# Kernel tuning notes

Hardware: AMD Instinct MI355X
Metric: run time of the kernel (lower is better)

The kernel has to match this reference:

```python
import jax, jax.numpy as jnp
import numpy as np

BN_EPS = 1e-5

# Binary activation with hardtanh STE semantics (forward: sign)
@jax.custom_vjp
def binary_act(x):
    return jnp.sign(x)

def _ba_fwd(x):
    return jnp.sign(x), x

def _ba_bwd(x, g):
    return (jnp.where(jnp.abs(x) > 1.0, 0.0, g),)

binary_act.defvjp(_ba_fwd, _ba_bwd)

# Binary weight quantizer (forward: sign, backward: identity STE)
@jax.custom_vjp
def binary_w(x):
    return jnp.sign(x)

def _bw_fwd(x):
    return jnp.sign(x), None

def _bw_bwd(_, g):
    return (g,)

binary_w.defvjp(_bw_fwd, _bw_bwd)


def setup_inputs() -> dict:
    key = jax.random.key(0)
    k1, k2, k3 = jax.random.split(key, 3)
    B, C_in, H, W_sp = 32, 256, 56, 56
    C_out, KH, KW = 256, 3, 3
    x = jax.random.normal(k1, (B, C_in, H, W_sp), dtype=jnp.float32)
    weight = jax.random.normal(k2, (C_out, C_in, KH, KW), dtype=jnp.float32) * 0.05
    bias = jax.random.normal(k3, (C_out,), dtype=jnp.float32) * 0.01
    gamma = jnp.ones((C_out,), dtype=jnp.float32)
    beta = jnp.zeros((C_out,), dtype=jnp.float32)
    return {"x": x, "weight": weight, "bias": bias, "gamma": gamma, "beta": beta}


def reference(x, weight, bias, gamma, beta):
    # --- activation binarization (A=2): sign ---
    xb = binary_act(x)
    # --- weight binarization (W=2): mean-center over in-channel dim, clamp, sign * alpha ---
    wc = weight - jnp.mean(weight, axis=1, keepdims=True)
    wc = jnp.clip(wc, -1.0, 1.0)
    alpha = jnp.mean(jnp.abs(wc), axis=(1, 2, 3), keepdims=True)  # per-output-channel scale
    wq = binary_w(wc) * alpha
    # --- conv2d, stride 1, padding 1 ---
    y = jax.lax.conv_general_dilated(
        xb, wq, window_strides=(1, 1), padding=((1, 1), (1, 1)),
        dimension_numbers=("NCHW", "OIHW", "NCHW"))
    y = y + bias[None, :, None, None]
    # --- BatchNorm2d (training-mode batch statistics, biased variance) ---
    mu = jnp.mean(y, axis=(0, 2, 3), keepdims=True)
    var = jnp.var(y, axis=(0, 2, 3), keepdims=True)
    y = (y - mu) * jax.lax.rsqrt(var + BN_EPS)
    y = y * gamma[None, :, None, None] + beta[None, :, None, None]
    # --- last_relu=1 ---
    y = jax.nn.relu(y)
    # --- last_bin=1 (A=2 -> binary activation) ---
    y = binary_act(y)
    return y
```

## Files before the change

kernel.cpp:

```cpp
#include <hip/hip_runtime.h>

typedef unsigned long long u64;
typedef int i32x4 __attribute__((ext_vector_type(4)));
typedef int i32x16 __attribute__((ext_vector_type(16)));

#define N_SP 3136
#define C_IN 256
#define C_OUT 256
#define BATCH 32
#define NBLK 896
#define XROW 64
#define XPLANE (58 * XROW * 256)
#define XSIZE ((size_t)BATCH * XPLANE)

__global__ __launch_bounds__(256) void prep_weights(const float* __restrict__ w,
                                                    char* __restrict__ A_pack,
                                                    double* __restrict__ alpha) {
    const int o = blockIdx.x;
    const int i = threadIdx.x;
    const int lane = i & 63, wvid = i >> 6;
    __shared__ double part[4][9];
    __shared__ double part2[4];

    float wv[9];
    const float* wp = w + ((size_t)o * C_IN + i) * 9;
#pragma unroll
    for (int t = 0; t < 9; ++t) wv[t] = wp[t];

#pragma unroll
    for (int t = 0; t < 9; ++t) {
        double v = (double)wv[t];
#pragma unroll
        for (int off = 32; off > 0; off >>= 1) v += __shfl_down(v, off);
        if (lane == 0) part[wvid][t] = v;
    }
    __syncthreads();

    double asum = 0.0;
#pragma unroll
    for (int t = 0; t < 9; ++t) {
        double mean = (part[0][t] + part[1][t] + part[2][t] + part[3][t]) * (1.0 / 256.0);
        double wc = (double)wv[t] - mean;
        int idx16 = ((t * 8 + (i >> 5)) * 8 + (o >> 5)) * 64 + (((i >> 4) & 1) << 5) + (o & 31);
        A_pack[(size_t)idx16 * 16 + (i & 15)] = (char)(wc > 0.0 ? 1 : -1);
        double aw = fabs(wc);
        if (aw > 1.0) aw = 1.0;
        asum += aw;
    }
#pragma unroll
    for (int off = 32; off > 0; off >>= 1) asum += __shfl_down(asum, off);
    if (lane == 0) part2[wvid] = asum;
    __syncthreads();
    if (i == 0)
        alpha[o] = (part2[0] + part2[1] + part2[2] + part2[3]) * (1.0 / 2304.0);
}

__global__ __launch_bounds__(256) void sign_transpose(const float* __restrict__ x,
                                                      char* __restrict__ xsT) {
    const int sp0 = blockIdx.x * 64;
    const int b = blockIdx.y;
    const int lane = threadIdx.x & 63;
    const int wv = threadIdx.x >> 6;
    __shared__ char tile[64 * 272];

    {
        const int tidl = (blockIdx.y * 49 + blockIdx.x) * 256 + threadIdx.x;
        if (tidl < 294912) {
            const int bb = tidl / 9216;
            const int r = tidl - bb * 9216;
            int hp, wp, c16;
            if (r < 2048) {
                hp = (r >> 10) * 57;
                wp = (r >> 4) & 63;
                c16 = (r & 15) << 4;
            } else {
                int r2 = r - 2048;
                hp = 1 + (r2 >> 7);
                int q = r2 & 127;
                int wi = q >> 4;
                wp = (wi == 0) ? 0 : 56 + wi;
                c16 = (q & 15) << 4;
            }
            *(i32x4*)(xsT + (((size_t)(bb * 58 + hp) << 6) + wp) * 256 + c16) =
                (i32x4){0, 0, 0, 0};
        }
    }

    const float* xp = x + ((size_t)(b * 256 + (wv << 6))) * N_SP + sp0 + lane;
#pragma unroll
    for (int q = 0; q < 4; ++q) {
        unsigned d[4];
#pragma unroll
        for (int dd = 0; dd < 4; ++dd) {
            unsigned v = 0;
#pragma unroll
            for (int kk = 0; kk < 4; ++kk) {
                int ci_l = (q << 4) + (dd << 2) + kk;
                float xv = xp[(size_t)ci_l * N_SP];
                v |= (unsigned)(xv > 0.0f ? 0x01u : 0xFFu) << (8 * kk);
            }
            d[dd] = v;
        }
        *(i32x4*)(tile + lane * 272 + (wv << 6) + (q << 4)) =
            (i32x4){(int)d[0], (int)d[1], (int)d[2], (int)d[3]};
    }
    __syncthreads();

    const int t = threadIdx.x;
#pragma unroll
    for (int j = 0; j < 4; ++j) {
        int sp_loc = (j << 4) + (t >> 4);
        int ci0 = (t & 15) << 4;
        i32x4 v = *(const i32x4*)(tile + sp_loc * 272 + ci0);
        int spg = sp0 + sp_loc;
        int h = spg / 56, w = spg - h * 56;
        size_t dst = (((size_t)(b * 58 + h + 1) << 6) + (w + 1)) * 256 + ci0;
        *(i32x4*)(xsT + dst) = v;
    }
}

__global__ __launch_bounds__(256, 2) void conv_mfma(const char* __restrict__ xsT,
                                                    const char* __restrict__ A_pack,
                                                    float* __restrict__ out,
                                                    int2* __restrict__ partials) {
    const int tid = threadIdx.x;
    const int lane = tid & 63;
    const int wv = tid >> 6;
    const int l31 = lane & 31, l5 = lane >> 5;
    const int blk = blockIdx.x;
    const int b = blk / 28;
    const int h0 = (blk - b * 28) * 2;

    __shared__ char slab[4 * 58 * 272];

    {
        const char* src = xsT + ((size_t)(b * 58 + h0) << 6) * 256;
        for (int c = tid; c < 4 * 58 * 16; c += 256) {
            int dh = c / (58 * 16);
            int rem = c - dh * (58 * 16);
            int wp = rem >> 4, c16 = (rem & 15) << 4;
            *(i32x4*)(slab + (dh * 58 + wp) * 272 + c16) =
                *(const i32x4*)(src + (size_t)dh * (XROW * 256) + wp * 256 + c16);
        }
    }
    __syncthreads();

    i32x16 acc[2][2][2] = {};

    const char* apb = A_pack + ((size_t)(2 * wv * 64 + lane)) * 16;
    const char* sb0 = slab + l31 * 272 + l5 * 16;
    int w1_0 = 32 + l31;     if (w1_0 > 57) w1_0 = 57;
    int w1_1 = 33 + l31;     if (w1_1 > 57) w1_1 = 57;
    int w1_2 = 34 + l31;     if (w1_2 > 57) w1_2 = 57;
    const char* sb1_0 = slab + w1_0 * 272 + l5 * 16;
    const char* sb1_1 = slab + w1_1 * 272 + l5 * 16;
    const char* sb1_2 = slab + w1_2 * 272 + l5 * 16;

#pragma unroll
    for (int tap = 0; tap < 9; ++tap) {
        const int dh = tap / 3, dw = tap - 3 * (tap / 3);
        const char* sb1 = (dw == 0) ? sb1_0 : ((dw == 1) ? sb1_1 : sb1_2);
#pragma unroll
        for (int cib = 0; cib < 8; ++cib) {
            const int it = tap * 8 + cib;
            i32x4 a0 = *(const i32x4*)(apb + (size_t)it * 8192);
            i32x4 a1 = *(const i32x4*)(apb + (size_t)it * 8192 + 1024);
            i32x4 b00 = *(const i32x4*)(sb0 + ((dh + 0) * 58 + dw) * 272 + cib * 32);
            i32x4 b01 = *(const i32x4*)(sb0 + ((dh + 1) * 58 + dw) * 272 + cib * 32);
            i32x4 b10 = *(const i32x4*)(sb1 + (dh + 0) * 58 * 272 + cib * 32);
            i32x4 b11 = *(const i32x4*)(sb1 + (dh + 1) * 58 * 272 + cib * 32);
            acc[0][0][0] = __builtin_amdgcn_mfma_i32_32x32x32_i8(a0, b00, acc[0][0][0], 0, 0, 0);
            acc[0][0][1] = __builtin_amdgcn_mfma_i32_32x32x32_i8(a0, b01, acc[0][0][1], 0, 0, 0);
            acc[0][1][0] = __builtin_amdgcn_mfma_i32_32x32x32_i8(a0, b10, acc[0][1][0], 0, 0, 0);
            acc[0][1][1] = __builtin_amdgcn_mfma_i32_32x32x32_i8(a0, b11, acc[0][1][1], 0, 0, 0);
            acc[1][0][0] = __builtin_amdgcn_mfma_i32_32x32x32_i8(a1, b00, acc[1][0][0], 0, 0, 0);
            acc[1][0][1] = __builtin_amdgcn_mfma_i32_32x32x32_i8(a1, b01, acc[1][0][1], 0, 0, 0);
            acc[1][1][0] = __builtin_amdgcn_mfma_i32_32x32x32_i8(a1, b10, acc[1][1][0], 0, 0, 0);
            acc[1][1][1] = __builtin_amdgcn_mfma_i32_32x32x32_i8(a1, b11, acc[1][1][1], 0, 0, 0);
        }
    }

    float* ob = out + ((size_t)(b * 256)) * N_SP + h0 * 56;
#pragma unroll
    for (int co_i = 0; co_i < 2; ++co_i) {
        const int co5 = 2 * wv + co_i;
#pragma unroll
        for (int nh = 0; nh < 2; ++nh) {
            const int w = nh * 32 + l31;
            if (w < 56) {
#pragma unroll
                for (int row = 0; row < 2; ++row)
#pragma unroll
                    for (int reg = 0; reg < 16; ++reg) {
                        int corow = (reg & 3) + 8 * (reg >> 2) + 4 * l5;
                        ob[(size_t)(co5 * 32 + corow) * N_SP + row * 56 + w] =
                            (float)acc[co_i][nh][row][reg];
                    }
            }
        }
    }

    __syncthreads();
    int* sp_s = (int*)slab;
    int* sp_q = (int*)slab + 256;
#pragma unroll
    for (int co_i = 0; co_i < 2; ++co_i) {
#pragma unroll
        for (int reg = 0; reg < 16; ++reg) {
            int v00 = acc[co_i][0][0][reg], v01 = acc[co_i][0][1][reg];
            int v10 = (l31 < 24) ? acc[co_i][1][0][reg] : 0;
            int v11 = (l31 < 24) ? acc[co_i][1][1][reg] : 0;
            int s = v00 + v01 + v10 + v11;
            unsigned q = (unsigned)(v00 * v00) + (unsigned)(v01 * v01)
                       + (unsigned)(v10 * v10) + (unsigned)(v11 * v11);
#pragma unroll
            for (int off = 16; off > 0; off >>= 1) {
                s += __shfl_xor(s, off);
                q += (unsigned)__shfl_xor((int)q, off);
            }
            if (l31 == 0) {
                int corow = (reg & 3) + 8 * (reg >> 2) + 4 * l5;
                sp_s[(2 * wv + co_i) * 32 + corow] = s;
                sp_q[(2 * wv + co_i) * 32 + corow] = (int)q;
            }
        }
    }
    __syncthreads();
    partials[(size_t)tid * NBLK + blk] = make_int2(sp_s[tid], sp_q[tid]);
}

__global__ __launch_bounds__(256) void stats_consts(const int2* __restrict__ partials,
                                                    const double* __restrict__ alpha,
                                                    const float* __restrict__ gamma,
                                                    const float* __restrict__ beta,
                                                    double* __restrict__ AB) {
    const int c = blockIdx.x;
    const int t = threadIdx.x;
    long long s1 = 0, s2 = 0;
    for (int blk = t; blk < NBLK; blk += 256) {
        int2 v = partials[(size_t)c * NBLK + blk];
        s1 += v.x;
        s2 += (long long)v.y;
    }
#pragma unroll
    for (int off = 32; off > 0; off >>= 1) {
        s1 += __shfl_down(s1, off);
        s2 += __shfl_down(s2, off);
    }
    __shared__ long long p1[4], p2[4];
    if ((t & 63) == 0) { p1[t >> 6] = s1; p2[t >> 6] = s2; }
    __syncthreads();
    if (t == 0) {
        double S1 = (double)(p1[0] + p1[1] + p1[2] + p1[3]);
        double S2 = (double)(p2[0] + p2[1] + p2[2] + p2[3]);
        const double N = (double)(BATCH * N_SP);
        double mu = S1 / N;
        double var = S2 / N - mu * mu;
        double a = alpha[c];
        double vy = a * a * var;
        double scale = (double)gamma[c] / sqrt(vy + 1e-5);
        double A = a * scale;
        double B = (double)beta[c] - A * mu;
        AB[c] = A;
        AB[C_OUT + c] = B;
    }
}

__global__ __launch_bounds__(256) void finalize(float* __restrict__ out,
                                                const double* __restrict__ AB) {
    const unsigned i4 = blockIdx.x * 256 + threadIdx.x;
    const unsigned e = i4 << 2;
    const int c = (int)((e / N_SP) & (C_OUT - 1));
    const double A = AB[c];
    const double B = AB[C_OUT + c];
    float4 v = ((float4*)out)[i4];
    v.x = (A * (double)v.x + B) > 0.0 ? 1.0f : 0.0f;
    v.y = (A * (double)v.y + B) > 0.0 ? 1.0f : 0.0f;
    v.z = (A * (double)v.z + B) > 0.0 ? 1.0f : 0.0f;
    v.w = (A * (double)v.w + B) > 0.0 ? 1.0f : 0.0f;
    ((float4*)out)[i4] = v;
}

extern "C" void kernel_launch(void* const* d_in, const int* in_sizes, int n_in,
                              void* d_out, int out_size, void* d_ws, size_t ws_size,
                              hipStream_t stream) {
    const float* x      = (const float*)d_in[0];
    const float* weight = (const float*)d_in[1];
    const float* bias   = (const float*)d_in[2];   (void)bias;
    const float* gamma  = (const float*)d_in[3];
    const float* beta   = (const float*)d_in[4];
    float* out = (float*)d_out;

    char* ws = (char*)d_ws;
    double* alpha = (double*)(ws + 4096);
    double* AB    = (double*)(ws + 8192);
    char*   A_pack = (char*)(ws + 16384);
    int2*   partials = (int2*)(ws + (1 << 20));
    char*   xsT   = (char*)(ws + (5 << 20));

    prep_weights<<<C_OUT, 256, 0, stream>>>(weight, A_pack, alpha);
    sign_transpose<<<dim3(49, BATCH), 256, 0, stream>>>(x, xsT);
    conv_mfma<<<dim3(NBLK), 256, 0, stream>>>(xsT, A_pack, out, partials);
    stats_consts<<<C_OUT, 256, 0, stream>>>(partials, alpha, gamma, beta, AB);
    finalize<<<(out_size / 4) / 256, 256, 0, stream>>>(out, AB);
}
```

Before: 357.0 us.

## Store conv results as int16 intermediate and finalize from compact buffer

The conv kernel now writes its integer accumulators as 16-bit shorts into a workspace buffer instead of fp32 into the output. A new finalize kernel reads the shorts and writes the binarized fp32 output, so the intermediate round trip moves about half as many bytes. This only happens when the workspace is large enough; otherwise the old fp32 path runs. Launch bounds on the conv kernel also change from 2 to 1 blocks per CU, which may lower occupancy. The int16 cast relies on accumulators fitting in 16 bits (at most 2304 in magnitude).

```diff
diff --git a/kernel.cpp b/kernel.cpp
--- a/kernel.cpp
+++ b/kernel.cpp
@@ -3,6 +3,7 @@
 typedef unsigned long long u64;
 typedef int i32x4 __attribute__((ext_vector_type(4)));
 typedef int i32x16 __attribute__((ext_vector_type(16)));
+typedef short s16x8 __attribute__((ext_vector_type(8)));
 
 #define N_SP 3136
 #define C_IN 256
@@ -12,6 +13,8 @@
 #define XROW 64
 #define XPLANE (58 * XROW * 256)
 #define XSIZE ((size_t)BATCH * XPLANE)
+#define S16_OFF ((size_t)36 << 20)
+#define S16_BYTES ((size_t)BATCH * C_OUT * N_SP * 2)
 
 __global__ __launch_bounds__(256) void prep_weights(const float* __restrict__ w,
                                                     char* __restrict__ A_pack,
@@ -119,9 +122,10 @@
     }
 }
 
-__global__ __launch_bounds__(256, 2) void conv_mfma(const char* __restrict__ xsT,
+__global__ __launch_bounds__(256, 1) void conv_mfma(const char* __restrict__ xsT,
                                                     const char* __restrict__ A_pack,
                                                     float* __restrict__ out,
+                                                    short* __restrict__ s16,
                                                     int2* __restrict__ partials) {
     const int tid = threadIdx.x;
     const int lane = tid & 63;
@@ -180,22 +184,44 @@
         }
     }
 
-    float* ob = out + ((size_t)(b * 256)) * N_SP + h0 * 56;
-#pragma unroll
-    for (int co_i = 0; co_i < 2; ++co_i) {
-        const int co5 = 2 * wv + co_i;
-#pragma unroll
-        for (int nh = 0; nh < 2; ++nh) {
-            const int w = nh * 32 + l31;
-            if (w < 56) {
-#pragma unroll
-                for (int row = 0; row < 2; ++row)
-#pragma unroll
-                    for (int reg = 0; reg < 16; ++reg) {
-                        int corow = (reg & 3) + 8 * (reg >> 2) + 4 * l5;
-                        ob[(size_t)(co5 * 32 + corow) * N_SP + row * 56 + w] =
-                            (float)acc[co_i][nh][row][reg];
-                    }
+    if (s16) {
+        short* sb = s16 + ((size_t)(b * 256)) * N_SP + h0 * 56;
+#pragma unroll
+        for (int co_i = 0; co_i < 2; ++co_i) {
+            const int co5 = 2 * wv + co_i;
+#pragma unroll
+            for (int nh = 0; nh < 2; ++nh) {
+                const int w = nh * 32 + l31;
+                if (w < 56) {
+#pragma unroll
+                    for (int row = 0; row < 2; ++row)
+#pragma unroll
+                        for (int reg = 0; reg < 16; ++reg) {
+                            int corow = (reg & 3) + 8 * (reg >> 2) + 4 * l5;
+                            sb[(size_t)(co5 * 32 + corow) * N_SP + row * 56 + w] =
+                                (short)acc[co_i][nh][row][reg];
+                        }
+                }
+            }
+        }
+    } else {
+        float* ob = out + ((size_t)(b * 256)) * N_SP + h0 * 56;
+#pragma unroll
+        for (int co_i = 0; co_i < 2; ++co_i) {
+            const int co5 = 2 * wv + co_i;
+#pragma unroll
+            for (int nh = 0; nh < 2; ++nh) {
+                const int w = nh * 32 + l31;
+                if (w < 56) {
+#pragma unroll
+                    for (int row = 0; row < 2; ++row)
+#pragma unroll
+                        for (int reg = 0; reg < 16; ++reg) {
+                            int corow = (reg & 3) + 8 * (reg >> 2) + 4 * l5;
+                            ob[(size_t)(co5 * 32 + corow) * N_SP + row * 56 + w] =
+                                (float)acc[co_i][nh][row][reg];
+                        }
+                }
             }
         }
     }
@@ -281,6 +307,28 @@
     ((float4*)out)[i4] = v;
 }
 
+__global__ __launch_bounds__(256) void finalize16(const short* __restrict__ S,
+                                                  float* __restrict__ out,
+                                                  const double* __restrict__ AB) {
+    const unsigned t = blockIdx.x * 256 + threadIdx.x;
+    const unsigned e = t << 3;
+    const int c = (int)((e / N_SP) & (C_OUT - 1));
+    const double A = AB[c];
+    const double B = AB[C_OUT + c];
+    s16x8 v = *(const s16x8*)(S + e);
+    float4 o0, o1;
+    o0.x = (A * (double)v[0] + B) > 0.0 ? 1.0f : 0.0f;
+    o0.y = (A * (double)v[1] + B) > 0.0 ? 1.0f : 0.0f;
+    o0.z = (A * (double)v[2] + B) > 0.0 ? 1.0f : 0.0f;
+    o0.w = (A * (double)v[3] + B) > 0.0 ? 1.0f : 0.0f;
+    o1.x = (A * (double)v[4] + B) > 0.0 ? 1.0f : 0.0f;
+    o1.y = (A * (double)v[5] + B) > 0.0 ? 1.0f : 0.0f;
+    o1.z = (A * (double)v[6] + B) > 0.0 ? 1.0f : 0.0f;
+    o1.w = (A * (double)v[7] + B) > 0.0 ? 1.0f : 0.0f;
+    *(float4*)(out + e) = o0;
+    *(float4*)(out + e + 4) = o1;
+}
+
 extern "C" void kernel_launch(void* const* d_in, const int* in_sizes, int n_in,
                               void* d_out, int out_size, void* d_ws, size_t ws_size,
                               hipStream_t stream) {
@@ -297,10 +345,15 @@
     char*   A_pack = (char*)(ws + 16384);
     int2*   partials = (int2*)(ws + (1 << 20));
     char*   xsT   = (char*)(ws + (5 << 20));
+    const bool use16 = ws_size >= S16_OFF + S16_BYTES;
+    short*  s16 = use16 ? (short*)(ws + S16_OFF) : (short*)0;
 
     prep_weights<<<C_OUT, 256, 0, stream>>>(weight, A_pack, alpha);
     sign_transpose<<<dim3(49, BATCH), 256, 0, stream>>>(x, xsT);
-    conv_mfma<<<dim3(NBLK), 256, 0, stream>>>(xsT, A_pack, out, partials);
+    conv_mfma<<<dim3(NBLK), 256, 0, stream>>>(xsT, A_pack, out, s16, partials);
     stats_consts<<<C_OUT, 256, 0, stream>>>(partials, alpha, gamma, beta, AB);
-    finalize<<<(out_size / 4) / 256, 256, 0, stream>>>(out, AB);
-}
+    if (use16)
+        finalize16<<<12544, 256, 0, stream>>>(s16, out, AB);
+    else
+        finalize<<<(out_size / 4) / 256, 256, 0, stream>>>(out, AB);
+}
```

Result: no change. 361.3 us (+1.2%).
